# Performance work log

Hardware: AMD Instinct MI355X
Metric: run time of the kernel (lower is better)

The kernel has to match this reference:

```python
import jax, jax.numpy as jnp
import numpy as np

B, S, D, H, L, TPB = 4, 1020, 1024, 16, 4, 17
VOBS, VACT = 4096, 16
DH = D // H
EPS = 1e-3  # keras LayerNormalization default epsilon


def _ln(x, g, b):
    m = jnp.mean(x, axis=-1, keepdims=True)
    v = jnp.mean((x - m) ** 2, axis=-1, keepdims=True)
    return (x - m) * jax.lax.rsqrt(v + EPS) * g + b


def setup_inputs() -> dict:
    key = jax.random.key(0)
    ks = iter(jax.random.split(key, 64))
    def p(shape, s=0.02):
        return jax.random.normal(next(ks), shape, jnp.float32) * s
    pos = np.arange(S)
    is_obs = jnp.asarray((pos % TPB) < (TPB - 1))
    tok = jax.random.randint(next(ks), (B, S), 0, VOBS)
    tok = jnp.where(is_obs[None, :], tok, tok % VACT).astype(jnp.int32)
    d = dict(
        tokens=tok,
        pos_emb=p((S, D)), emb_obs=p((VOBS, D)), emb_act=p((VACT, D)),
        ln1_g=jnp.ones((L, D)), ln1_b=jnp.zeros((L, D)),
        wq=p((L, D, D)), bq=jnp.zeros((L, D)),
        wk=p((L, D, D)), bk=jnp.zeros((L, D)),
        wv=p((L, D, D)), bv=jnp.zeros((L, D)),
        wo=p((L, D, D)), bo=jnp.zeros((L, D)),
        ln2_g=jnp.ones((L, D)), ln2_b=jnp.zeros((L, D)),
        w1=p((L, D, 4 * D)), b1=jnp.zeros((L, 4 * D)),
        w2=p((L, 4 * D, D)), b2=jnp.zeros((L, D)),
        lnf_g=jnp.ones((D,)), lnf_b=jnp.zeros((D,)),
        ho1=p((D, D)), bo1=jnp.zeros((D,)),
        ho2=p((D, VOBS)), bo2=jnp.zeros((VOBS,)),
        he1=p((D, D)), be1=jnp.zeros((D,)),
        he2=p((D, 2)), be2=jnp.zeros((2,)),
    )
    return d


def reference(tokens, pos_emb, emb_obs, emb_act, ln1_g, ln1_b, wq, bq, wk, bk,
              wv, bv, wo, bo, ln2_g, ln2_b, w1, b1, w2, b2, lnf_g, lnf_b,
              ho1, bo1, ho2, bo2, he1, be1, he2, be2):
    pos = jnp.arange(S)
    is_obs = (pos % TPB) < (TPB - 1)  # obs positions within each block
    # token embedding: obs table on obs positions, act table on act positions
    x = jnp.where(is_obs[None, :, None],
                  emb_obs[jnp.minimum(tokens, VOBS - 1)],
                  emb_act[jnp.minimum(tokens, VACT - 1)])
    x = x + pos_emb[None]
    neg_mask = (1.0 - jnp.tril(jnp.ones((S, S), jnp.float32))) * -1e9
    inv_sqrt_dk = 1.0 / np.sqrt(DH).astype(np.float32)
    for i in range(L):
        h = _ln(x, ln1_g[i], ln1_b[i])
        q = (h @ wq[i] + bq[i]).reshape(B, S, H, DH).transpose(0, 2, 1, 3)
        k = (h @ wk[i] + bk[i]).reshape(B, S, H, DH).transpose(0, 2, 1, 3)
        v = (h @ wv[i] + bv[i]).reshape(B, S, H, DH).transpose(0, 2, 1, 3)
        scores = jnp.einsum('bhqd,bhkd->bhqk', q, k) * inv_sqrt_dk + neg_mask
        w = jax.nn.softmax(scores, axis=-1)
        o = jnp.einsum('bhqk,bhkd->bhqd', w, v).transpose(0, 2, 1, 3).reshape(B, S, D)
        x = x + (o @ wo[i] + bo[i])
        h = _ln(x, ln2_g[i], ln2_b[i])
        h = jax.nn.gelu(h @ w1[i] + b1[i], approximate=False) @ w2[i] + b2[i]
        x = x + h
    x = _ln(x, lnf_g, lnf_b)
    # head slices (static)
    p_np = np.arange(S)
    head_obs_idx = jnp.asarray(np.nonzero(((p_np + 1) % TPB) != (TPB - 1))[0])  # 960
    act_idx = jnp.asarray(np.nonzero((p_np % TPB) == (TPB - 1))[0])            # 60
    xo = x[:, head_obs_idx]
    logits_obs = jax.nn.relu(xo @ ho1 + bo1) @ ho2 + bo2   # [B, 960, VOBS]
    xe = x[:, act_idx]
    logits_ends = jax.nn.relu(xe @ he1 + be1) @ he2 + be2  # [B, 60, 2]
    return (logits_obs, logits_ends)
```

## Files before the change

### kernel.cpp

```cpp
#include <hip/hip_runtime.h>
#include <hip/hip_bf16.h>
#include <math.h>

namespace {

constexpr int kS = 1020, kD = 1024, kTPB = 17, kDH = 64;
constexpr int kVOBS = 4096, kVACT = 16;
constexpr int kBS = 4080;
constexpr float kEPS = 1e-3f;

typedef float f32x4 __attribute__((ext_vector_type(4)));
typedef __bf16 bfx8 __attribute__((ext_vector_type(8)));
typedef unsigned short u16;
typedef u16 us8 __attribute__((ext_vector_type(8)));
typedef u16 us4 __attribute__((ext_vector_type(4)));

__device__ __forceinline__ float bf2f(u16 u) {
  union { unsigned int i; float f; } v; v.i = (unsigned int)u << 16; return v.f;
}
__device__ __forceinline__ u16 f2bf(float f) {
  union { float f; unsigned int i; } v; v.f = f;
  unsigned int r = v.i + 0x7FFFu + ((v.i >> 16) & 1u);
  return (u16)(r >> 16);
}

__global__ void k_embed(const int* __restrict__ tokens, const float* __restrict__ pos_emb,
                        const float* __restrict__ emb_obs, const float* __restrict__ emb_act,
                        float* __restrict__ x) {
  int bs = blockIdx.x;
  int s = bs % kS;
  int tk = tokens[bs];
  bool obs = (s % kTPB) < (kTPB - 1);
  const float* e;
  if (obs) { int t2 = tk < kVOBS - 1 ? tk : kVOBS - 1; e = emb_obs + (size_t)t2 * kD; }
  else     { int t2 = tk < kVACT - 1 ? tk : kVACT - 1; e = emb_act + (size_t)t2 * kD; }
  int c = threadIdx.x * 4;
  float4 ev = *(const float4*)(e + c);
  float4 pv = *(const float4*)(pos_emb + (size_t)s * kD + c);
  float4 o; o.x = ev.x + pv.x; o.y = ev.y + pv.y; o.z = ev.z + pv.z; o.w = ev.w + pv.w;
  *(float4*)(x + (size_t)bs * kD + c) = o;
}

__global__ void k_pack_bias(const float* __restrict__ bq, const float* __restrict__ bk,
                            const float* __restrict__ bv, float* __restrict__ bqkv) {
  int idx = blockIdx.x * 256 + threadIdx.x;
  int l = idx / 3072, rem = idx % 3072;
  int sel = rem >> 10, cc = rem & 1023;
  const float* src = sel == 0 ? bq : (sel == 1 ? bk : bv);
  bqkv[idx] = src[l * kD + cc];
}

__global__ void k_ln(const float* __restrict__ x, const float* __restrict__ g,
                     const float* __restrict__ b, u16* __restrict__ out) {
  int row = blockIdx.x;
  int t = threadIdx.x;
  const float* xr = x + (size_t)row * kD;
  float4 v = *(const float4*)(xr + t * 4);
  float s1 = v.x + v.y + v.z + v.w;
  float s2 = v.x * v.x + v.y * v.y + v.z * v.z + v.w * v.w;
  #pragma unroll
  for (int m = 32; m; m >>= 1) { s1 += __shfl_xor(s1, m); s2 += __shfl_xor(s2, m); }
  __shared__ float ls1[4], ls2[4];
  int w = t >> 6;
  if ((t & 63) == 0) { ls1[w] = s1; ls2[w] = s2; }
  __syncthreads();
  float S1 = ls1[0] + ls1[1] + ls1[2] + ls1[3];
  float S2 = ls2[0] + ls2[1] + ls2[2] + ls2[3];
  float mean = S1 * (1.0f / kD);
  float var = S2 * (1.0f / kD) - mean * mean;
  float rs = rsqrtf(var + kEPS);
  int c = t * 4;
  float4 gv = *(const float4*)(g + c);
  float4 bv = *(const float4*)(b + c);
  us4 o;
  o[0] = f2bf((v.x - mean) * rs * gv.x + bv.x);
  o[1] = f2bf((v.y - mean) * rs * gv.y + bv.y);
  o[2] = f2bf((v.z - mean) * rs * gv.z + bv.z);
  o[3] = f2bf((v.w - mean) * rs * gv.w + bv.w);
  *(us4*)(out + (size_t)row * kD + c) = o;
}

__global__ void k_transpose(const float* __restrict__ in, u16* __restrict__ out,
                            int R, int C, int ld) {
  __shared__ float tile[32][33];
  int tx = threadIdx.x, ty = threadIdx.y;
  int c0 = blockIdx.x * 32, r0 = blockIdx.y * 32;
  #pragma unroll
  for (int i = 0; i < 4; ++i)
    tile[ty + i * 8][tx] = in[(size_t)(r0 + ty + i * 8) * ld + c0 + tx];
  __syncthreads();
  #pragma unroll
  for (int i = 0; i < 4; ++i)
    out[(size_t)(c0 + ty + i * 8) * R + r0 + tx] = f2bf(tile[tx][ty + i * 8]);
}

struct T4 {
  const float* in0; const float* in1; const float* in2; const float* in3;
  u16* out0; u16* out1; u16* out2; u16* out3;
  int ld;
};
__global__ void k_transpose4(T4 sp) {
  const float* in; u16* out;
  switch (blockIdx.z) {
    case 0:  in = sp.in0; out = sp.out0; break;
    case 1:  in = sp.in1; out = sp.out1; break;
    case 2:  in = sp.in2; out = sp.out2; break;
    default: in = sp.in3; out = sp.out3; break;
  }
  __shared__ float tile[32][33];
  int tx = threadIdx.x, ty = threadIdx.y;
  int c0 = blockIdx.x * 32, r0 = blockIdx.y * 32;
  #pragma unroll
  for (int i = 0; i < 4; ++i)
    tile[ty + i * 8][tx] = in[(size_t)(r0 + ty + i * 8) * sp.ld + c0 + tx];
  __syncthreads();
  #pragma unroll
  for (int i = 0; i < 4; ++i)
    out[(size_t)(c0 + ty + i * 8) * 1024 + r0 + tx] = f2bf(tile[tx][ty + i * 8]);
}

template <int EPI>
__global__ void __launch_bounds__(512, 2)
k_gemm256(const u16* __restrict__ A, const u16* __restrict__ Bt, const float* __restrict__ bias,
          void* __restrict__ out, int M, int K, int ldo) {
  __shared__ alignas(16) u16 As[2][256 * 64];
  __shared__ alignas(16) u16 Bs[2][256 * 64];
  const int tid = threadIdx.x;
  const int lane = tid & 63, wv = tid >> 6;
  const int wm = wv >> 2, wn = wv & 3;
  const int m0 = blockIdx.x * 256, n0 = blockIdx.y * 256;
  f32x4 acc[8][4] = {};

  auto stageIter = [&](int buf, int k0, int it) {
    int u = (it & 3) * 512 + tid;
    int row = u >> 3, g = u & 7;
    int gsw = g ^ (row & 7);
    int grow;
    const u16* srcBase;
    u16* dstBase;
    if (it < 4) {
      grow = m0 + row; if (grow >= M) grow = M - 1;
      srcBase = A; dstBase = &As[buf][0];
    } else {
      grow = n0 + row;
      srcBase = Bt; dstBase = &Bs[buf][0];
    }
    const u16* src = srcBase + (size_t)grow * K + k0 + gsw * 8;
    u16* dst = dstBase + ((it & 3) * 512 + wv * 64) * 8;
    __builtin_amdgcn_global_load_lds(
        (const __attribute__((address_space(1))) unsigned int*)src,
        (__attribute__((address_space(3))) unsigned int*)dst, 16, 0, 0);
  };

  const int nt = K >> 6;
  #pragma unroll
  for (int it = 0; it < 8; ++it) stageIter(0, 0, it);

  for (int t = 0; t < nt; ++t) {
    const int pb = t & 1;
    const int k0n = (t + 1) << 6;
    const bool pf = (t + 1 < nt);
    asm volatile("s_waitcnt vmcnt(0)" ::: "memory");
    __builtin_amdgcn_s_barrier();
    __builtin_amdgcn_sched_barrier(0);

    #pragma unroll
    for (int kh = 0; kh < 2; ++kh) {
      bfx8 bfr[4], afr[4];
      #pragma unroll
      for (int n = 0; n < 4; ++n) {
        int row = wn * 64 + n * 16 + (lane & 15);
        bfr[n] = *(const bfx8*)(&Bs[pb][row * 64 + ((((kh << 2) + (lane >> 4)) ^ (row & 7)) << 3)]);
      }
      #pragma unroll
      for (int j = 0; j < 4; ++j) {
        int row = wm * 128 + j * 16 + (lane & 15);
        afr[j] = *(const bfx8*)(&As[pb][row * 64 + ((((kh << 2) + (lane >> 4)) ^ (row & 7)) << 3)]);
      }
      if (pf) { stageIter(pb ^ 1, k0n, kh * 4 + 0); stageIter(pb ^ 1, k0n, kh * 4 + 1); }
      __builtin_amdgcn_s_barrier();
      asm volatile("s_waitcnt lgkmcnt(0)" ::: "memory");
      __builtin_amdgcn_sched_barrier(0);
      __builtin_amdgcn_s_setprio(1);
      #pragma unroll
      for (int j = 0; j < 4; ++j)
        #pragma unroll
        for (int n = 0; n < 4; ++n)
          acc[j][n] = __builtin_amdgcn_mfma_f32_16x16x32_bf16(afr[j], bfr[n], acc[j][n], 0, 0, 0);
      __builtin_amdgcn_s_setprio(0);
      __builtin_amdgcn_s_barrier();

      #pragma unroll
      for (int j = 0; j < 4; ++j) {
        int row = wm * 128 + 64 + j * 16 + (lane & 15);
        afr[j] = *(const bfx8*)(&As[pb][row * 64 + ((((kh << 2) + (lane >> 4)) ^ (row & 7)) << 3)]);
      }
      if (pf) { stageIter(pb ^ 1, k0n, kh * 4 + 2); stageIter(pb ^ 1, k0n, kh * 4 + 3); }
      __builtin_amdgcn_s_barrier();
      asm volatile("s_waitcnt lgkmcnt(0)" ::: "memory");
      __builtin_amdgcn_sched_barrier(0);
      __builtin_amdgcn_s_setprio(1);
      #pragma unroll
      for (int j = 0; j < 4; ++j)
        #pragma unroll
        for (int n = 0; n < 4; ++n)
          acc[4 + j][n] = __builtin_amdgcn_mfma_f32_16x16x32_bf16(afr[j], bfr[n], acc[4 + j][n], 0, 0, 0);
      __builtin_amdgcn_s_setprio(0);
      __builtin_amdgcn_s_barrier();
    }
  }

  #pragma unroll
  for (int jf = 0; jf < 8; ++jf) {
    #pragma unroll
    for (int n = 0; n < 4; ++n) {
      int gcol = n0 + wn * 64 + n * 16 + (lane & 15);
      float bv = bias ? bias[gcol] : 0.0f;
      #pragma unroll
      for (int r = 0; r < 4; ++r) {
        int grow = m0 + wm * 128 + jf * 16 + (lane >> 4) * 4 + r;
        if (grow >= M) continue;
        float val = acc[jf][n][r] + bv;
        size_t o2 = (size_t)grow * ldo + gcol;
        if (EPI == 0) {
          ((u16*)out)[o2] = f2bf(val);
        } else if (EPI == 2) {
          ((u16*)out)[o2] = f2bf(0.5f * val * (1.f + erff(val * 0.70710678118654752440f)));
        } else {
          ((float*)out)[o2] = val;
        }
      }
    }
  }
}

template <int EPI, int BM>
__global__ void __launch_bounds__(256)
k_gemm(const u16* __restrict__ A, const u16* __restrict__ Bt, const float* __restrict__ bias,
       const float* __restrict__ resid, void* __restrict__ out, int M, int N, int K, int ldo) {
  constexpr int MFRAG = BM / 32;
  constexpr int LOADS = BM / 64 + 2;
  __shared__ alignas(16) u16 As[3][BM * 32];
  __shared__ alignas(16) u16 Bs[3][128 * 32];
  int tid = threadIdx.x;
  int m0 = blockIdx.x * BM, n0 = blockIdx.y * 128;
  int lane = tid & 63, wv = tid >> 6;
  int wm = wv >> 1, wn = wv & 1;
  f32x4 acc[MFRAG][4] = {};

  auto stage = [&](int buf, int k0) {
    #pragma unroll
    for (int n = 0; n < BM / 64; ++n) {
      int u = n * 256 + tid;
      int r = u >> 2, ch = u & 3;
      int gr = m0 + r; if (gr >= M) gr = M - 1;
      int cg = ch ^ ((r >> 1) & 3);
      const u16* src = A + (size_t)gr * K + k0 + cg * 8;
      __builtin_amdgcn_global_load_lds(
          (const __attribute__((address_space(1))) unsigned int*)src,
          (__attribute__((address_space(3))) unsigned int*)&As[buf][(n * 256 + wv * 64) * 8],
          16, 0, 0);
    }
    #pragma unroll
    for (int n = 0; n < 2; ++n) {
      int u = n * 256 + tid;
      int r = u >> 2, ch = u & 3;
      int cg = ch ^ ((r >> 1) & 3);
      const u16* src = Bt + (size_t)(n0 + r) * K + k0 + cg * 8;
      __builtin_amdgcn_global_load_lds(
          (const __attribute__((address_space(1))) unsigned int*)src,
          (__attribute__((address_space(3))) unsigned int*)&Bs[buf][(n * 256 + wv * 64) * 8],
          16, 0, 0);
    }
  };

  const int nk = K >> 5;
  stage(0, 0);
  stage(1, 32);
  stage(2, 64);
  for (int t = 0; t < nk; ++t) {
    int cur = t % 3;
    if (t + 2 < nk)
      asm volatile("s_waitcnt vmcnt(%0)" :: "i"(2 * LOADS) : "memory");
    else if (t + 1 < nk)
      asm volatile("s_waitcnt vmcnt(%0)" :: "i"(LOADS) : "memory");
    else
      asm volatile("s_waitcnt vmcnt(0)" ::: "memory");
    __builtin_amdgcn_s_barrier();
    __builtin_amdgcn_sched_barrier(0);

    bfx8 af[MFRAG], bfr[4];
    int ch = lane >> 4;
    #pragma unroll
    for (int mf = 0; mf < MFRAG; ++mf) {
      int row = wm * (BM / 2) + mf * 16 + (lane & 15);
      af[mf] = *(const bfx8*)(&As[cur][row * 32 + ((ch ^ ((row >> 1) & 3)) << 3)]);
    }
    #pragma unroll
    for (int nf = 0; nf < 4; ++nf) {
      int row = wn * 64 + nf * 16 + (lane & 15);
      bfr[nf] = *(const bfx8*)(&Bs[cur][row * 32 + ((ch ^ ((row >> 1) & 3)) << 3)]);
    }
    asm volatile("s_waitcnt lgkmcnt(0)" ::: "memory");
    __builtin_amdgcn_s_barrier();
    __builtin_amdgcn_sched_barrier(0);
    if (t + 3 < nk) stage(cur, (t + 3) << 5);

    #pragma unroll
    for (int mf = 0; mf < MFRAG; ++mf)
      #pragma unroll
      for (int nf = 0; nf < 4; ++nf)
        acc[mf][nf] = __builtin_amdgcn_mfma_f32_16x16x32_bf16(af[mf], bfr[nf], acc[mf][nf], 0, 0, 0);
  }

  #pragma unroll
  for (int mf = 0; mf < MFRAG; ++mf) {
    #pragma unroll
    for (int nf = 0; nf < 4; ++nf) {
      int gcol = n0 + wn * 64 + nf * 16 + (lane & 15);
      float bv = bias ? bias[gcol] : 0.0f;
      #pragma unroll
      for (int r = 0; r < 4; ++r) {
        int grow = m0 + wm * (BM / 2) + mf * 16 + (lane >> 4) * 4 + r;
        if (grow >= M) continue;
        float val = acc[mf][nf][r] + bv;
        size_t off2 = (size_t)grow * ldo + gcol;
        if (EPI == 0) {
          ((u16*)out)[off2] = f2bf(val);
        } else if (EPI == 1) {
          ((u16*)out)[off2] = f2bf(val > 0.f ? val : 0.f);
        } else if (EPI == 2) {
          ((u16*)out)[off2] = f2bf(0.5f * val * (1.f + erff(val * 0.70710678118654752440f)));
        } else if (EPI == 3) {
          ((float*)out)[off2] = resid[off2] + val;
        } else {
          ((float*)out)[off2] = val;
        }
      }
    }
  }
}

__device__ __forceinline__ int swz(int row, int colu16) {
  return (row * 64 + colu16) ^ ((row & 7) << 3) ^ ((row & 24) << 1);
}

__global__ void __launch_bounds__(256)
k_attn(const u16* __restrict__ q, const u16* __restrict__ k, const u16* __restrict__ v,
       u16* __restrict__ o, int ldin) {
  __shared__ u16 Kl[64 * 64];
  __shared__ u16 Vt[64 * 64];
  const int qb = blockIdx.x * 64;
  const int bh = blockIdx.y;
  const int b = bh >> 4, hh = bh & 15;
  const int tid = threadIdx.x;
  const int lane = tid & 63, w = tid >> 6;
  const int g = lane >> 4, c = lane & 15;
  const int q0 = qb + w * 16;
  const size_t base = (size_t)(b * kS) * ldin + hh * kDH;

  bfx8 qf0, qf1;
  {
    int qr = q0 + c; if (qr >= kS) qr = kS - 1;
    const u16* qp = q + base + (size_t)qr * ldin + g * 8;
    qf0 = *(const bfx8*)(qp);
    qf1 = *(const bfx8*)(qp + 32);
  }

  float mst = -1e30f, lsum = 0.f;
  f32x4 ot[4] = {};

  const int ntiles = blockIdx.x + 1;
  for (int t = 0; t < ntiles; ++t) {
    const int kt = t * 64;
    {
      int kr = tid >> 2, ds2 = (tid & 3) * 16;
      int kg = kt + kr; if (kg >= kS) kg = kS - 1;
      const u16* kp = k + base + (size_t)kg * ldin + ds2;
      us8 a0 = *(const us8*)(kp);
      us8 a1 = *(const us8*)(kp + 8);
      *(us8*)(&Kl[swz(kr, ds2)]) = a0;
      *(us8*)(&Kl[swz(kr, ds2 + 8)]) = a1;
      const u16* vp = v + base + (size_t)kg * ldin + ds2;
      us8 b0 = *(const us8*)(vp);
      us8 b1 = *(const us8*)(vp + 8);
      #pragma unroll
      for (int i2 = 0; i2 < 8; ++i2) Vt[swz(ds2 + i2, kr)] = b0[i2];
      #pragma unroll
      for (int i2 = 0; i2 < 8; ++i2) Vt[swz(ds2 + 8 + i2, kr)] = b1[i2];
    }
    __syncthreads();

    f32x4 s[4];
    #pragma unroll
    for (int kb = 0; kb < 4; ++kb) {
      bfx8 kf0 = *(const bfx8*)(&Kl[swz(kb * 16 + c, g * 8)]);
      bfx8 kf1 = *(const bfx8*)(&Kl[swz(kb * 16 + c, g * 8 + 32)]);
      f32x4 acc = {};
      acc = __builtin_amdgcn_mfma_f32_16x16x32_bf16(kf0, qf0, acc, 0, 0, 0);
      acc = __builtin_amdgcn_mfma_f32_16x16x32_bf16(kf1, qf1, acc, 0, 0, 0);
      s[kb] = acc;
    }

    const int qg = q0 + c;
    const bool diag = (kt + 63 > q0);
    float p[4][4];
    float tmax = -1e30f;
    #pragma unroll
    for (int kb = 0; kb < 4; ++kb)
      #pragma unroll
      for (int r = 0; r < 4; ++r) {
        float val = s[kb][r] * 0.125f;
        if (diag && (kt + kb * 16 + g * 4 + r > qg)) val = -1e30f;
        p[kb][r] = val;
        tmax = fmaxf(tmax, val);
      }
    tmax = fmaxf(tmax, __shfl_xor(tmax, 16));
    tmax = fmaxf(tmax, __shfl_xor(tmax, 32));
    float mnew = fmaxf(mst, tmax);
    float alpha = __expf(mst - mnew);
    float psum = 0.f;
    #pragma unroll
    for (int kb = 0; kb < 4; ++kb)
      #pragma unroll
      for (int r = 0; r < 4; ++r) {
        float e = __expf(p[kb][r] - mnew);
        p[kb][r] = e;
        psum += e;
      }
    psum += __shfl_xor(psum, 16);
    psum += __shfl_xor(psum, 32);
    lsum = lsum * alpha + psum;
    mst = mnew;
    #pragma unroll
    for (int db = 0; db < 4; ++db) {
      ot[db][0] *= alpha; ot[db][1] *= alpha;
      ot[db][2] *= alpha; ot[db][3] *= alpha;
    }

    #pragma unroll
    for (int h = 0; h < 2; ++h) {
      bfx8 pf;
      #pragma unroll
      for (int j = 0; j < 8; ++j)
        pf[j] = (__bf16)p[2 * h + (j >> 2)][j & 3];
      #pragma unroll
      for (int db = 0; db < 4; ++db) {
        us4 lo = *(const us4*)(&Vt[swz(16 * db + c, 32 * h + 4 * g)]);
        us4 hi = *(const us4*)(&Vt[swz(16 * db + c, 32 * h + 16 + 4 * g)]);
        union { us8 u; bfx8 bf; } cv;
        cv.u[0] = lo[0]; cv.u[1] = lo[1]; cv.u[2] = lo[2]; cv.u[3] = lo[3];
        cv.u[4] = hi[0]; cv.u[5] = hi[1]; cv.u[6] = hi[2]; cv.u[7] = hi[3];
        ot[db] = __builtin_amdgcn_mfma_f32_16x16x32_bf16(cv.bf, pf, ot[db], 0, 0, 0);
      }
    }
    __syncthreads();
  }

  if (q0 + c < kS) {
    float inv = 1.0f / lsum;
    u16* op = o + (size_t)(b * kS) * kD + hh * kDH + (size_t)(q0 + c) * kD;
    #pragma unroll
    for (int db = 0; db < 4; ++db)
      #pragma unroll
      for (int r = 0; r < 4; ++r)
        op[16 * db + 4 * g + r] = f2bf(ot[db][r] * inv);
  }
}

__global__ void k_gather_obs(const u16* __restrict__ xf, u16* __restrict__ xo) {
  int r = blockIdx.x;
  int b = r / 960, rr = r % 960;
  int j = rr & 15, blk = rr >> 4;
  int s = blk * kTPB + j + (j == 15 ? 1 : 0);
  const unsigned int* src = (const unsigned int*)(xf + ((size_t)(b * kS + s)) * kD);
  unsigned int* dst = (unsigned int*)(xo + (size_t)r * kD);
  dst[threadIdx.x] = src[threadIdx.x];
  dst[threadIdx.x + 256] = src[threadIdx.x + 256];
}
__global__ void k_gather_act(const u16* __restrict__ xf, u16* __restrict__ xe) {
  int r = blockIdx.x;
  int b = r / 60, rr = r % 60;
  int s = rr * kTPB + (kTPB - 1);
  const unsigned int* src = (const unsigned int*)(xf + ((size_t)(b * kS + s)) * kD);
  unsigned int* dst = (unsigned int*)(xe + (size_t)r * kD);
  dst[threadIdx.x] = src[threadIdx.x];
  dst[threadIdx.x + 256] = src[threadIdx.x + 256];
}

__global__ void k_ends(const u16* __restrict__ t2, const float* __restrict__ he2,
                       const float* __restrict__ be2, float* __restrict__ out) {
  int r = blockIdx.x;
  int t = threadIdx.x;
  float p0 = 0.f, p1 = 0.f;
  for (int j = t; j < kD; j += 256) {
    float xv = bf2f(t2[(size_t)r * kD + j]);
    p0 += xv * he2[j * 2];
    p1 += xv * he2[j * 2 + 1];
  }
  #pragma unroll
  for (int msk = 32; msk; msk >>= 1) { p0 += __shfl_xor(p0, msk); p1 += __shfl_xor(p1, msk); }
  __shared__ float l0[4], l1[4];
  int w = t >> 6;
  if ((t & 63) == 0) { l0[w] = p0; l1[w] = p1; }
  __syncthreads();
  if (t == 0) {
    out[r * 2 + 0] = l0[0] + l0[1] + l0[2] + l0[3] + be2[0];
    out[r * 2 + 1] = l1[0] + l1[1] + l1[2] + l1[3] + be2[1];
  }
}

}

extern "C" void kernel_launch(void* const* d_in, const int* in_sizes, int n_in,
                              void* d_out, int out_size, void* d_ws, size_t ws_size,
                              hipStream_t stream) {
  const int*   tokens  = (const int*)  d_in[0];
  const float* pos_emb = (const float*)d_in[1];
  const float* emb_obs = (const float*)d_in[2];
  const float* emb_act = (const float*)d_in[3];
  const float* ln1_g = (const float*)d_in[4];
  const float* ln1_b = (const float*)d_in[5];
  const float* wq = (const float*)d_in[6];
  const float* bq = (const float*)d_in[7];
  const float* wk = (const float*)d_in[8];
  const float* bk = (const float*)d_in[9];
  const float* wv = (const float*)d_in[10];
  const float* bv = (const float*)d_in[11];
  const float* wo = (const float*)d_in[12];
  const float* bo = (const float*)d_in[13];
  const float* ln2_g = (const float*)d_in[14];
  const float* ln2_b = (const float*)d_in[15];
  const float* w1 = (const float*)d_in[16];
  const float* b1 = (const float*)d_in[17];
  const float* w2 = (const float*)d_in[18];
  const float* b2 = (const float*)d_in[19];
  const float* lnf_g = (const float*)d_in[20];
  const float* lnf_b = (const float*)d_in[21];
  const float* ho1 = (const float*)d_in[22];
  const float* bo1 = (const float*)d_in[23];
  const float* ho2 = (const float*)d_in[24];
  const float* bo2 = (const float*)d_in[25];
  const float* he1 = (const float*)d_in[26];
  const float* be1 = (const float*)d_in[27];
  const float* he2 = (const float*)d_in[28];
  const float* be2 = (const float*)d_in[29];
  (void)in_sizes; (void)n_in; (void)out_size; (void)ws_size;

  char* ws = (char*)d_ws;
  size_t off = 0;
  auto alloc = [&](size_t bytes) -> char* {
    char* p = ws + off; off += (bytes + 255) & ~(size_t)255; return p;
  };
  u16*   wTbig = (u16*)alloc((size_t)4096 * 1024 * 2);
  u16*   w2T   = (u16*)alloc((size_t)1024 * 4096 * 2);
  float* x  = (float*)alloc((size_t)kBS * kD * 4);
  u16*   h  = (u16*)alloc((size_t)kBS * kD * 2);
  char*  scr = alloc((size_t)kBS * 4096 * 2);
  float* bqkv = (float*)alloc((size_t)4 * 3072 * 4);
  const size_t slotB = (size_t)kBS * kD * 2;
  u16* qkv = (u16*)scr;
  u16* ob  = (u16*)(scr + (size_t)kBS * 3072 * 2);
  u16* mid = (u16*)scr;
  u16* xf = (u16*)scr;
  u16* xo = (u16*)(scr + slotB);
  u16* t1 = (u16*)(scr + 2 * slotB);
  u16* xe = (u16*)(scr + 3 * slotB);
  u16* t2 = (u16*)(scr + 3 * slotB + (size_t)240 * kD * 2 + 256);

  dim3 tb(32, 8);
  dim3 tg(32, 32);
  k_embed<<<kBS, 256, 0, stream>>>(tokens, pos_emb, emb_obs, emb_act, x);
  k_pack_bias<<<48, 256, 0, stream>>>(bq, bk, bv, bqkv);

  const size_t MB1 = (size_t)1024 * 1024;
  for (int i = 0; i < 4; ++i) {
    const size_t wOff = (size_t)i * kD * kD;
    k_ln<<<kBS, 256, 0, stream>>>(x, ln1_g + i * kD, ln1_b + i * kD, h);

    {
      T4 sp{wq + wOff, wk + wOff, wv + wOff, wo + wOff,
            wTbig, wTbig + MB1, wTbig + 2 * MB1, wTbig + 3 * MB1, 1024};
      k_transpose4<<<dim3(32, 32, 4), tb, 0, stream>>>(sp);
    }
    k_gemm256<0><<<dim3(16, 12), 512, 0, stream>>>(h, wTbig, bqkv + i * 3072, qkv,
                                                   kBS, 1024, 3072);

    k_attn<<<dim3(16, 64), 256, 0, stream>>>(qkv, qkv + 1024, qkv + 2048, ob, 3072);

    k_gemm<3, 64><<<dim3(64, 8), 256, 0, stream>>>(ob, wTbig + 3 * MB1, bo + i * kD, x, x,
                                                   kBS, 1024, 1024, 1024);

    k_ln<<<kBS, 256, 0, stream>>>(x, ln2_g + i * kD, ln2_b + i * kD, h);

    {
      const float* w1b = w1 + (size_t)i * kD * 4096;
      T4 sp{w1b, w1b + 1024, w1b + 2048, w1b + 3072,
            wTbig, wTbig + MB1, wTbig + 2 * MB1, wTbig + 3 * MB1, 4096};
      k_transpose4<<<dim3(32, 32, 4), tb, 0, stream>>>(sp);
    }
    k_transpose<<<dim3(32, 128), tb, 0, stream>>>(w2 + (size_t)i * 4096 * kD, w2T,
                                                  4096, 1024, 1024);
    k_gemm256<2><<<dim3(16, 16), 512, 0, stream>>>(h, wTbig, b1 + (size_t)i * 4096,
                                                   mid, kBS, 1024, 4096);
    k_gemm<3, 64><<<dim3(64, 8), 256, 0, stream>>>(mid, w2T, b2 + i * kD, x, x,
                                                   kBS, 1024, 4096, 1024);
  }

  k_ln<<<kBS, 256, 0, stream>>>(x, lnf_g, lnf_b, xf);
  k_gather_obs<<<3840, 256, 0, stream>>>(xf, xo);
  k_gather_act<<<240, 256, 0, stream>>>(xf, xe);

  k_transpose<<<tg, tb, 0, stream>>>(ho1, wTbig, 1024, 1024, 1024);
  k_gemm<1, 64><<<dim3(60, 8), 256, 0, stream>>>(xo, wTbig, bo1, nullptr, t1,
                                                 3840, 1024, 1024, 1024);
  k_transpose<<<tg, tb, 0, stream>>>(he1, w2T, 1024, 1024, 1024);
  {
    T4 sp{ho2, ho2 + 1024, ho2 + 2048, ho2 + 3072,
          wTbig, wTbig + MB1, wTbig + 2 * MB1, wTbig + 3 * MB1, 4096};
    k_transpose4<<<dim3(32, 32, 4), tb, 0, stream>>>(sp);
  }
  k_gemm256<4><<<dim3(15, 16), 512, 0, stream>>>(t1, wTbig, bo2,
                                                 (float*)d_out, 3840, 1024, 4096);
  k_gemm<1, 64><<<dim3(4, 8), 256, 0, stream>>>(xe, w2T, be1, nullptr, t2,
                                                240, 1024, 1024, 1024);
  k_ends<<<240, 256, 0, stream>>>(t2, he2, be2, (float*)d_out + (size_t)3840 * 4096);
}
```

Baseline: 1.266 ms.

## Replace small GEMM with 128x128 double-buffered kernel, pre-transpose V, reverse attention order

Replaces the 64x128 triple-buffered GEMM with a 128x128 tile, BK=64, double-buffered kernel. It interleaves prefetch with LDS reads and raises wave priority around the MFMA blocks. This is used for the Wo, W2 and head GEMMs. It also adds a kernel that transposes V per head into a separate buffer, so attention loads V rows with vector loads instead of scattered scalar LDS writes. Attention blocks are also launched in reverse order so the longest causal tiles start first. The extra transpose kernel costs another launch and extra memory traffic, and the larger GEMM tiles halve the grid size, which may lower occupancy on the small-M launches.

```diff
diff --git a/kernel.cpp b/kernel.cpp
--- a/kernel.cpp
+++ b/kernel.cpp
@@ -119,6 +119,25 @@
     out[(size_t)(c0 + ty + i * 8) * 1024 + r0 + tx] = f2bf(tile[tx][ty + i * 8]);
 }
 
+__global__ void k_vtrans(const u16* __restrict__ qkv, u16* __restrict__ vt) {
+  __shared__ u16 tile[32][33];
+  int bh = blockIdx.z; int b = bh >> 4, hh = bh & 15;
+  int s0 = blockIdx.x * 32, d0 = blockIdx.y * 32;
+  int tx = threadIdx.x, ty = threadIdx.y;
+  const u16* src = qkv + ((size_t)(b * kS)) * 3072 + 2048 + hh * 64;
+  #pragma unroll
+  for (int i = 0; i < 4; ++i) {
+    int s = s0 + ty + i * 8;
+    tile[ty + i * 8][tx] = (s < kS) ? src[(size_t)s * 3072 + d0 + tx] : (u16)0;
+  }
+  __syncthreads();
+  if (s0 + tx < kS) {
+    #pragma unroll
+    for (int i = 0; i < 4; ++i)
+      vt[((size_t)bh * 64 + d0 + ty + i * 8) * kS + s0 + tx] = tile[tx][ty + i * 8];
+  }
+}
+
 template <int EPI>
 __global__ void __launch_bounds__(512, 2)
 k_gemm256(const u16* __restrict__ A, const u16* __restrict__ Bt, const float* __restrict__ bias,
@@ -234,107 +253,98 @@
   }
 }
 
-template <int EPI, int BM>
-__global__ void __launch_bounds__(256)
-k_gemm(const u16* __restrict__ A, const u16* __restrict__ Bt, const float* __restrict__ bias,
-       const float* __restrict__ resid, void* __restrict__ out, int M, int N, int K, int ldo) {
-  constexpr int MFRAG = BM / 32;
-  constexpr int LOADS = BM / 64 + 2;
-  __shared__ alignas(16) u16 As[3][BM * 32];
-  __shared__ alignas(16) u16 Bs[3][128 * 32];
-  int tid = threadIdx.x;
-  int m0 = blockIdx.x * BM, n0 = blockIdx.y * 128;
-  int lane = tid & 63, wv = tid >> 6;
-  int wm = wv >> 1, wn = wv & 1;
-  f32x4 acc[MFRAG][4] = {};
-
-  auto stage = [&](int buf, int k0) {
-    #pragma unroll
-    for (int n = 0; n < BM / 64; ++n) {
-      int u = n * 256 + tid;
-      int r = u >> 2, ch = u & 3;
-      int gr = m0 + r; if (gr >= M) gr = M - 1;
-      int cg = ch ^ ((r >> 1) & 3);
-      const u16* src = A + (size_t)gr * K + k0 + cg * 8;
-      __builtin_amdgcn_global_load_lds(
-          (const __attribute__((address_space(1))) unsigned int*)src,
-          (__attribute__((address_space(3))) unsigned int*)&As[buf][(n * 256 + wv * 64) * 8],
-          16, 0, 0);
-    }
-    #pragma unroll
-    for (int n = 0; n < 2; ++n) {
-      int u = n * 256 + tid;
-      int r = u >> 2, ch = u & 3;
-      int cg = ch ^ ((r >> 1) & 3);
-      const u16* src = Bt + (size_t)(n0 + r) * K + k0 + cg * 8;
-      __builtin_amdgcn_global_load_lds(
-          (const __attribute__((address_space(1))) unsigned int*)src,
-          (__attribute__((address_space(3))) unsigned int*)&Bs[buf][(n * 256 + wv * 64) * 8],
-          16, 0, 0);
-    }
+template <int EPI>
+__global__ void __launch_bounds__(256, 2)
+k_gemm128(const u16* __restrict__ A, const u16* __restrict__ Bt, const float* __restrict__ bias,
+          const float* __restrict__ resid, void* __restrict__ out, int M, int K, int ldo) {
+  __shared__ alignas(16) u16 As[2][128 * 64];
+  __shared__ alignas(16) u16 Bs[2][128 * 64];
+  const int tid = threadIdx.x;
+  const int lane = tid & 63, wv = tid >> 6;
+  const int wm = wv >> 1, wn = wv & 1;
+  const int m0 = blockIdx.x * 128, n0 = blockIdx.y * 128;
+  f32x4 acc[4][4] = {};
+
+  auto stageIter = [&](int buf, int k0, int it) {
+    int u = (it & 3) * 256 + tid;
+    int row = u >> 3, g = u & 7;
+    int gsw = g ^ (row & 7);
+    int grow;
+    const u16* srcBase;
+    u16* dstBase;
+    if (it < 4) {
+      grow = m0 + row; if (grow >= M) grow = M - 1;
+      srcBase = A; dstBase = &As[buf][0];
+    } else {
+      grow = n0 + row;
+      srcBase = Bt; dstBase = &Bs[buf][0];
+    }
+    const u16* src = srcBase + (size_t)grow * K + k0 + gsw * 8;
+    u16* dst = dstBase + ((it & 3) * 256 + wv * 64) * 8;
+    __builtin_amdgcn_global_load_lds(
+        (const __attribute__((address_space(1))) unsigned int*)src,
+        (__attribute__((address_space(3))) unsigned int*)dst, 16, 0, 0);
   };
 
-  const int nk = K >> 5;
-  stage(0, 0);
-  stage(1, 32);
-  stage(2, 64);
-  for (int t = 0; t < nk; ++t) {
-    int cur = t % 3;
-    if (t + 2 < nk)
-      asm volatile("s_waitcnt vmcnt(%0)" :: "i"(2 * LOADS) : "memory");
-    else if (t + 1 < nk)
-      asm volatile("s_waitcnt vmcnt(%0)" :: "i"(LOADS) : "memory");
-    else
-      asm volatile("s_waitcnt vmcnt(0)" ::: "memory");
+  const int nt = K >> 6;
+  #pragma unroll
+  for (int it = 0; it < 8; ++it) stageIter(0, 0, it);
+
+  for (int t = 0; t < nt; ++t) {
+    const int pb = t & 1;
+    const int k0n = (t + 1) << 6;
+    const bool pf = (t + 1 < nt);
+    asm volatile("s_waitcnt vmcnt(0)" ::: "memory");
     __builtin_amdgcn_s_barrier();
     __builtin_amdgcn_sched_barrier(0);
 
-    bfx8 af[MFRAG], bfr[4];
-    int ch = lane >> 4;
-    #pragma unroll
-    for (int mf = 0; mf < MFRAG; ++mf) {
-      int row = wm * (BM / 2) + mf * 16 + (lane & 15);
-      af[mf] = *(const bfx8*)(&As[cur][row * 32 + ((ch ^ ((row >> 1) & 3)) << 3)]);
-    }
-    #pragma unroll
-    for (int nf = 0; nf < 4; ++nf) {
-      int row = wn * 64 + nf * 16 + (lane & 15);
-      bfr[nf] = *(const bfx8*)(&Bs[cur][row * 32 + ((ch ^ ((row >> 1) & 3)) << 3)]);
-    }
-    asm volatile("s_waitcnt lgkmcnt(0)" ::: "memory");
-    __builtin_amdgcn_s_barrier();
-    __builtin_amdgcn_sched_barrier(0);
-    if (t + 3 < nk) stage(cur, (t + 3) << 5);
-
-    #pragma unroll
-    for (int mf = 0; mf < MFRAG; ++mf)
-      #pragma unroll
-      for (int nf = 0; nf < 4; ++nf)
-        acc[mf][nf] = __builtin_amdgcn_mfma_f32_16x16x32_bf16(af[mf], bfr[nf], acc[mf][nf], 0, 0, 0);
-  }
-
-  #pragma unroll
-  for (int mf = 0; mf < MFRAG; ++mf) {
-    #pragma unroll
-    for (int nf = 0; nf < 4; ++nf) {
-      int gcol = n0 + wn * 64 + nf * 16 + (lane & 15);
+    #pragma unroll
+    for (int kh = 0; kh < 2; ++kh) {
+      bfx8 afr[4], bfr[4];
+      #pragma unroll
+      for (int j = 0; j < 4; ++j) {
+        int row = wm * 64 + j * 16 + (lane & 15);
+        afr[j] = *(const bfx8*)(&As[pb][row * 64 + ((((kh << 2) + (lane >> 4)) ^ (row & 7)) << 3)]);
+      }
+      #pragma unroll
+      for (int n = 0; n < 4; ++n) {
+        int row = wn * 64 + n * 16 + (lane & 15);
+        bfr[n] = *(const bfx8*)(&Bs[pb][row * 64 + ((((kh << 2) + (lane >> 4)) ^ (row & 7)) << 3)]);
+      }
+      if (pf) {
+        stageIter(pb ^ 1, k0n, kh * 4 + 0); stageIter(pb ^ 1, k0n, kh * 4 + 1);
+        stageIter(pb ^ 1, k0n, kh * 4 + 2); stageIter(pb ^ 1, k0n, kh * 4 + 3);
+      }
+      __builtin_amdgcn_s_barrier();
+      asm volatile("s_waitcnt lgkmcnt(0)" ::: "memory");
+      __builtin_amdgcn_sched_barrier(0);
+      __builtin_amdgcn_s_setprio(1);
+      #pragma unroll
+      for (int j = 0; j < 4; ++j)
+        #pragma unroll
+        for (int n = 0; n < 4; ++n)
+          acc[j][n] = __builtin_amdgcn_mfma_f32_16x16x32_bf16(afr[j], bfr[n], acc[j][n], 0, 0, 0);
+      __builtin_amdgcn_s_setprio(0);
+      __builtin_amdgcn_s_barrier();
+    }
+  }
+
+  #pragma unroll
+  for (int jf = 0; jf < 4; ++jf) {
+    #pragma unroll
+    for (int n = 0; n < 4; ++n) {
+      int gcol = n0 + wn * 64 + n * 16 + (lane & 15);
       float bv = bias ? bias[gcol] : 0.0f;
       #pragma unroll
       for (int r = 0; r < 4; ++r) {
-        int grow = m0 + wm * (BM / 2) + mf * 16 + (lane >> 4) * 4 + r;
+        int grow = m0 + wm * 64 + jf * 16 + (lane >> 4) * 4 + r;
         if (grow >= M) continue;
-        float val = acc[mf][nf][r] + bv;
-        size_t off2 = (size_t)grow * ldo + gcol;
-        if (EPI == 0) {
-          ((u16*)out)[off2] = f2bf(val);
-        } else if (EPI == 1) {
-          ((u16*)out)[off2] = f2bf(val > 0.f ? val : 0.f);
-        } else if (EPI == 2) {
-          ((u16*)out)[off2] = f2bf(0.5f * val * (1.f + erff(val * 0.70710678118654752440f)));
-        } else if (EPI == 3) {
-          ((float*)out)[off2] = resid[off2] + val;
+        float val = acc[jf][n][r] + bv;
+        size_t o2 = (size_t)grow * ldo + gcol;
+        if (EPI == 1) {
+          ((u16*)out)[o2] = f2bf(val > 0.f ? val : 0.f);
         } else {
-          ((float*)out)[off2] = val;
+          ((float*)out)[o2] = resid[o2] + val;
         }
       }
     }
@@ -346,11 +356,12 @@
 }
 
 __global__ void __launch_bounds__(256)
-k_attn(const u16* __restrict__ q, const u16* __restrict__ k, const u16* __restrict__ v,
+k_attn(const u16* __restrict__ q, const u16* __restrict__ k, const u16* __restrict__ vt,
        u16* __restrict__ o, int ldin) {
   __shared__ u16 Kl[64 * 64];
   __shared__ u16 Vt[64 * 64];
-  const int qb = blockIdx.x * 64;
+  const int qbi = gridDim.x - 1 - blockIdx.x;
+  const int qb = qbi * 64;
   const int bh = blockIdx.y;
   const int b = bh >> 4, hh = bh & 15;
   const int tid = threadIdx.x;
@@ -370,7 +381,7 @@
   float mst = -1e30f, lsum = 0.f;
   f32x4 ot[4] = {};
 
-  const int ntiles = blockIdx.x + 1;
+  const int ntiles = qbi + 1;
   for (int t = 0; t < ntiles; ++t) {
     const int kt = t * 64;
     {
@@ -381,13 +392,20 @@
       us8 a1 = *(const us8*)(kp + 8);
       *(us8*)(&Kl[swz(kr, ds2)]) = a0;
       *(us8*)(&Kl[swz(kr, ds2 + 8)]) = a1;
-      const u16* vp = v + base + (size_t)kg * ldin + ds2;
-      us8 b0 = *(const us8*)(vp);
-      us8 b1 = *(const us8*)(vp + 8);
-      #pragma unroll
-      for (int i2 = 0; i2 < 8; ++i2) Vt[swz(ds2 + i2, kr)] = b0[i2];
-      #pragma unroll
-      for (int i2 = 0; i2 < 8; ++i2) Vt[swz(ds2 + 8 + i2, kr)] = b1[i2];
+      const u16* vrow = vt + ((size_t)bh * 64 + kr) * kS;
+      if (kt + 64 <= kS) {
+        #pragma unroll
+        for (int j = 0; j < 4; ++j) {
+          us4 v4 = *(const us4*)(vrow + kt + ds2 + 4 * j);
+          *(us4*)(&Vt[swz(kr, ds2 + 4 * j)]) = v4;
+        }
+      } else {
+        #pragma unroll
+        for (int j = 0; j < 16; ++j) {
+          int cc = kt + ds2 + j; if (cc > kS - 1) cc = kS - 1;
+          Vt[swz(kr, ds2 + j)] = vrow[cc];
+        }
+      }
     }
     __syncthreads();
 
@@ -562,6 +580,7 @@
   u16* qkv = (u16*)scr;
   u16* ob  = (u16*)(scr + (size_t)kBS * 3072 * 2);
   u16* mid = (u16*)scr;
+  u16* vt  = h;
   u16* xf = (u16*)scr;
   u16* xo = (u16*)(scr + slotB);
   u16* t1 = (u16*)(scr + 2 * slotB);
@@ -586,10 +605,11 @@
     k_gemm256<0><<<dim3(16, 12), 512, 0, stream>>>(h, wTbig, bqkv + i * 3072, qkv,
                                                    kBS, 1024, 3072);
 
-    k_attn<<<dim3(16, 64), 256, 0, stream>>>(qkv, qkv + 1024, qkv + 2048, ob, 3072);
-
-    k_gemm<3, 64><<<dim3(64, 8), 256, 0, stream>>>(ob, wTbig + 3 * MB1, bo + i * kD, x, x,
-                                                   kBS, 1024, 1024, 1024);
+    k_vtrans<<<dim3(32, 2, 64), tb, 0, stream>>>(qkv, vt);
+    k_attn<<<dim3(16, 64), 256, 0, stream>>>(qkv, qkv + 1024, vt, ob, 3072);
+
+    k_gemm128<3><<<dim3(32, 8), 256, 0, stream>>>(ob, wTbig + 3 * MB1, bo + i * kD, x, x,
+                                                  kBS, 1024, 1024);
 
     k_ln<<<kBS, 256, 0, stream>>>(x, ln2_g + i * kD, ln2_b + i * kD, h);
 
@@ -603,8 +623,8 @@
                                                   4096, 1024, 1024);
     k_gemm256<2><<<dim3(16, 16), 512, 0, stream>>>(h, wTbig, b1 + (size_t)i * 4096,
                                                    mid, kBS, 1024, 4096);
-    k_gemm<3, 64><<<dim3(64, 8), 256, 0, stream>>>(mid, w2T, b2 + i * kD, x, x,
-                                                   kBS, 1024, 4096, 1024);
+    k_gemm128<3><<<dim3(32, 8), 256, 0, stream>>>(mid, w2T, b2 + i * kD, x, x,
+                                                  kBS, 4096, 1024);
   }
 
   k_ln<<<kBS, 256, 0, stream>>>(x, lnf_g, lnf_b, xf);
@@ -612,8 +632,8 @@
   k_gather_act<<<240, 256, 0, stream>>>(xf, xe);
 
   k_transpose<<<tg, tb, 0, stream>>>(ho1, wTbig, 1024, 1024, 1024);
-  k_gemm<1, 64><<<dim3(60, 8), 256, 0, stream>>>(xo, wTbig, bo1, nullptr, t1,
-                                                 3840, 1024, 1024, 1024);
+  k_gemm128<1><<<dim3(30, 8), 256, 0, stream>>>(xo, wTbig, bo1, nullptr, t1,
+                                                3840, 1024, 1024);
   k_transpose<<<tg, tb, 0, stream>>>(he1, w2T, 1024, 1024, 1024);
   {
     T4 sp{ho2, ho2 + 1024, ho2 + 2048, ho2 + 3072,
@@ -622,7 +642,7 @@
   }
   k_gemm256<4><<<dim3(15, 16), 512, 0, stream>>>(t1, wTbig, bo2,
                                                  (float*)d_out, 3840, 1024, 4096);
-  k_gemm<1, 64><<<dim3(4, 8), 256, 0, stream>>>(xe, w2T, be1, nullptr, t2,
-                                                240, 1024, 1024, 1024);
+  k_gemm128<1><<<dim3(2, 8), 256, 0, stream>>>(xe, w2T, be1, nullptr, t2,
+                                               240, 1024, 1024);
   k_ends<<<240, 256, 0, stream>>>(t2, he2, be2, (float*)d_out + (size_t)3840 * 4096);
 }
```

New measurement: 1.443 ms. +14.0%, slower.

## Pre-transpose V for attention, reverse causal block order, use 256-tile GEMM for FFN down

Applied to the files above, without the earlier changes.

Adds a kernel that transposes V per head into a [bh, d, s] buffer (reusing the h workspace), so attention loads V tiles with vector reads instead of scattered per-element transposed LDS writes. Attention blocks are launched in reverse query order so the longest causal tiles start first, which should balance load. The FFN down-projection moves from the 64x128 GEMM to the 256x256 kernel with a new residual-add epilogue, but that gives only 64 blocks, which may underfill the GPU. Unused epilogue branches in k_gemm are removed.

```diff
diff --git a/kernel.cpp b/kernel.cpp
--- a/kernel.cpp
+++ b/kernel.cpp
@@ -119,6 +119,25 @@
     out[(size_t)(c0 + ty + i * 8) * 1024 + r0 + tx] = f2bf(tile[tx][ty + i * 8]);
 }
 
+__global__ void k_vtrans(const u16* __restrict__ qkv, u16* __restrict__ vt) {
+  __shared__ u16 tile[32][33];
+  int bh = blockIdx.z; int b = bh >> 4, hh = bh & 15;
+  int s0 = blockIdx.x * 32, d0 = blockIdx.y * 32;
+  int tx = threadIdx.x, ty = threadIdx.y;
+  const u16* src = qkv + ((size_t)(b * kS)) * 3072 + 2048 + hh * 64;
+  #pragma unroll
+  for (int i = 0; i < 4; ++i) {
+    int s = s0 + ty + i * 8;
+    tile[ty + i * 8][tx] = (s < kS) ? src[(size_t)s * 3072 + d0 + tx] : (u16)0;
+  }
+  __syncthreads();
+  if (s0 + tx < kS) {
+    #pragma unroll
+    for (int i = 0; i < 4; ++i)
+      vt[((size_t)bh * 64 + d0 + ty + i * 8) * kS + s0 + tx] = tile[tx][ty + i * 8];
+  }
+}
+
 template <int EPI>
 __global__ void __launch_bounds__(512, 2)
 k_gemm256(const u16* __restrict__ A, const u16* __restrict__ Bt, const float* __restrict__ bias,
@@ -226,6 +245,8 @@
           ((u16*)out)[o2] = f2bf(val);
         } else if (EPI == 2) {
           ((u16*)out)[o2] = f2bf(0.5f * val * (1.f + erff(val * 0.70710678118654752440f)));
+        } else if (EPI == 3) {
+          ((float*)out)[o2] = ((float*)out)[o2] + val;
         } else {
           ((float*)out)[o2] = val;
         }
@@ -325,16 +346,10 @@
         if (grow >= M) continue;
         float val = acc[mf][nf][r] + bv;
         size_t off2 = (size_t)grow * ldo + gcol;
-        if (EPI == 0) {
-          ((u16*)out)[off2] = f2bf(val);
-        } else if (EPI == 1) {
+        if (EPI == 1) {
           ((u16*)out)[off2] = f2bf(val > 0.f ? val : 0.f);
-        } else if (EPI == 2) {
-          ((u16*)out)[off2] = f2bf(0.5f * val * (1.f + erff(val * 0.70710678118654752440f)));
-        } else if (EPI == 3) {
+        } else {
           ((float*)out)[off2] = resid[off2] + val;
-        } else {
-          ((float*)out)[off2] = val;
         }
       }
     }
@@ -346,11 +361,12 @@
 }
 
 __global__ void __launch_bounds__(256)
-k_attn(const u16* __restrict__ q, const u16* __restrict__ k, const u16* __restrict__ v,
+k_attn(const u16* __restrict__ q, const u16* __restrict__ k, const u16* __restrict__ vt,
        u16* __restrict__ o, int ldin) {
   __shared__ u16 Kl[64 * 64];
   __shared__ u16 Vt[64 * 64];
-  const int qb = blockIdx.x * 64;
+  const int qbi = gridDim.x - 1 - blockIdx.x;
+  const int qb = qbi * 64;
   const int bh = blockIdx.y;
   const int b = bh >> 4, hh = bh & 15;
   const int tid = threadIdx.x;
@@ -370,7 +386,7 @@
   float mst = -1e30f, lsum = 0.f;
   f32x4 ot[4] = {};
 
-  const int ntiles = blockIdx.x + 1;
+  const int ntiles = qbi + 1;
   for (int t = 0; t < ntiles; ++t) {
     const int kt = t * 64;
     {
@@ -381,13 +397,20 @@
       us8 a1 = *(const us8*)(kp + 8);
       *(us8*)(&Kl[swz(kr, ds2)]) = a0;
       *(us8*)(&Kl[swz(kr, ds2 + 8)]) = a1;
-      const u16* vp = v + base + (size_t)kg * ldin + ds2;
-      us8 b0 = *(const us8*)(vp);
-      us8 b1 = *(const us8*)(vp + 8);
-      #pragma unroll
-      for (int i2 = 0; i2 < 8; ++i2) Vt[swz(ds2 + i2, kr)] = b0[i2];
-      #pragma unroll
-      for (int i2 = 0; i2 < 8; ++i2) Vt[swz(ds2 + 8 + i2, kr)] = b1[i2];
+      const u16* vrow = vt + ((size_t)bh * 64 + kr) * kS;
+      if (kt + 64 <= kS) {
+        #pragma unroll
+        for (int j = 0; j < 4; ++j) {
+          us4 v4 = *(const us4*)(vrow + kt + ds2 + 4 * j);
+          *(us4*)(&Vt[swz(kr, ds2 + 4 * j)]) = v4;
+        }
+      } else {
+        #pragma unroll
+        for (int j = 0; j < 16; ++j) {
+          int cc = kt + ds2 + j; if (cc > kS - 1) cc = kS - 1;
+          Vt[swz(kr, ds2 + j)] = vrow[cc];
+        }
+      }
     }
     __syncthreads();
 
@@ -562,6 +585,7 @@
   u16* qkv = (u16*)scr;
   u16* ob  = (u16*)(scr + (size_t)kBS * 3072 * 2);
   u16* mid = (u16*)scr;
+  u16* vt  = h;
   u16* xf = (u16*)scr;
   u16* xo = (u16*)(scr + slotB);
   u16* t1 = (u16*)(scr + 2 * slotB);
@@ -586,7 +610,8 @@
     k_gemm256<0><<<dim3(16, 12), 512, 0, stream>>>(h, wTbig, bqkv + i * 3072, qkv,
                                                    kBS, 1024, 3072);
 
-    k_attn<<<dim3(16, 64), 256, 0, stream>>>(qkv, qkv + 1024, qkv + 2048, ob, 3072);
+    k_vtrans<<<dim3(32, 2, 64), tb, 0, stream>>>(qkv, vt);
+    k_attn<<<dim3(16, 64), 256, 0, stream>>>(qkv, qkv + 1024, vt, ob, 3072);
 
     k_gemm<3, 64><<<dim3(64, 8), 256, 0, stream>>>(ob, wTbig + 3 * MB1, bo + i * kD, x, x,
                                                    kBS, 1024, 1024, 1024);
@@ -603,8 +628,8 @@
                                                   4096, 1024, 1024);
     k_gemm256<2><<<dim3(16, 16), 512, 0, stream>>>(h, wTbig, b1 + (size_t)i * 4096,
                                                    mid, kBS, 1024, 4096);
-    k_gemm<3, 64><<<dim3(64, 8), 256, 0, stream>>>(mid, w2T, b2 + i * kD, x, x,
-                                                   kBS, 1024, 4096, 1024);
+    k_gemm256<3><<<dim3(16, 4), 512, 0, stream>>>(mid, w2T, b2 + i * kD, x,
+                                                  kBS, 4096, 1024);
   }
 
   k_ln<<<kBS, 256, 0, stream>>>(x, lnf_g, lnf_b, xf);
```

After: 1.626 ms. +28.4%, slower.
